# Performance work log

Measured on AMD Instinct MI355X. Metric: run time of the kernel, lower is better.

The kernel has to match this reference:

```python
import jax, jax.numpy as jnp
import numpy as np

B, N, C, H = 2, 2048, 1024, 16
HD = C // H
FF = 2 * C


def _layernorm(x, w, b, eps=1e-5):
    mu = jnp.mean(x, axis=-1, keepdims=True)
    var = jnp.var(x, axis=-1, keepdims=True)
    return (x - mu) * jax.lax.rsqrt(var + eps) * w + b


def setup_inputs() -> dict:
    key = jax.random.key(0)
    ks = jax.random.split(key, 16)
    std = 0.02
    d = {
        'q': jax.random.normal(ks[0], (B, N, C), jnp.float32),
        'k': jax.random.normal(ks[1], (B, N, C), jnp.float32),
        'v': jax.random.normal(ks[2], (B, N, C), jnp.float32),
        # attention projections (stored [in, out])
        'Wq': jax.random.normal(ks[3], (C, C), jnp.float32) * std,
        'bq': jnp.zeros((C,), jnp.float32),
        'Wk': jax.random.normal(ks[4], (C, C), jnp.float32) * std,
        'bk': jnp.zeros((C,), jnp.float32),
        'Wv': jax.random.normal(ks[5], (C, C), jnp.float32) * std,
        'bv': jnp.zeros((C,), jnp.float32),
        'Wo': jax.random.normal(ks[6], (C, C), jnp.float32) * std,
        'bo': jnp.zeros((C,), jnp.float32),
        # post-attention LayerNorm
        'ln_w': jnp.ones((C,), jnp.float32),
        'ln_b': jnp.zeros((C,), jnp.float32),
        # FFN
        'W1': jax.random.normal(ks[7], (C, FF), jnp.float32) * std,
        'b1': jnp.zeros((FF,), jnp.float32),
        'W2': jax.random.normal(ks[8], (FF, C), jnp.float32) * std,
        'b2': jnp.zeros((C,), jnp.float32),
    }
    return d


def reference(q, k, v, Wq, bq, Wk, bk, Wv, bv, Wo, bo, ln_w, ln_b, W1, b1, W2, b2):
    scale = HD ** -0.5
    # Note: the torch forward overwrites the normalized-input attention with
    # attention on raw q,k,v; only the second call affects the output.
    qh = (q @ Wq + bq).reshape(B, N, H, HD)  # [B,Nq,H,hd]
    kh = (k @ Wk + bk).reshape(B, N, H, HD)
    vh = (v @ Wv + bv).reshape(B, N, H, HD)
    attn = jnp.einsum('bqhd,bkhd->bhqk', qh, kh) * scale
    attn = jax.nn.softmax(attn, axis=-1)
    ctx = jnp.einsum('bhqk,bkhd->bqhd', attn, vh).reshape(B, N, C)
    x = ctx @ Wo + bo
    x = x + q  # residual (drop_path=0, dropout eval -> identity)
    h = _layernorm(x, ln_w, ln_b)
    y = jax.nn.gelu(h @ W1 + b1, approximate=False) @ W2 + b2
    return y + x
```

## Files before the change

### kernel.cpp

```cpp
#include <hip/hip_runtime.h>

constexpr int B_ = 2, N_ = 2048, C_ = 1024, H_ = 16, HD_ = 64, FF_ = 2048;

typedef __attribute__((ext_vector_type(8))) __bf16 bf16x8;
typedef __attribute__((ext_vector_type(4))) float f32x4;
typedef __attribute__((ext_vector_type(4))) short s16x4;

__device__ __forceinline__ unsigned short f2bf(float f) {
  union { float f; unsigned int u; } v; v.f = f;
  unsigned int r = v.u + 0x7fffu + ((v.u >> 16) & 1u);
  return (unsigned short)(r >> 16);
}

__device__ __forceinline__ void gload_lds16(const unsigned short* g, unsigned short* l) {
  __builtin_amdgcn_global_load_lds((const __attribute__((address_space(1))) void*)g,
                                   (__attribute__((address_space(3))) void*)l, 16, 0, 0);
}

__global__ __launch_bounds__(256)
void cast3_bf16(const float* __restrict__ q, const float* __restrict__ k,
                const float* __restrict__ v, unsigned short* __restrict__ qo,
                unsigned short* __restrict__ ko, unsigned short* __restrict__ vo, int n8) {
  int i = blockIdx.x * 256 + threadIdx.x;
  if (i >= n8) return;
  const float* in = blockIdx.z == 0 ? q : (blockIdx.z == 1 ? k : v);
  unsigned short* out = blockIdx.z == 0 ? qo : (blockIdx.z == 1 ? ko : vo);
  const float4 a = ((const float4*)in)[2 * i];
  const float4 b = ((const float4*)in)[2 * i + 1];
  uint4 o;
  o.x = (unsigned)f2bf(a.x) | ((unsigned)f2bf(a.y) << 16);
  o.y = (unsigned)f2bf(a.z) | ((unsigned)f2bf(a.w) << 16);
  o.z = (unsigned)f2bf(b.x) | ((unsigned)f2bf(b.y) << 16);
  o.w = (unsigned)f2bf(b.z) | ((unsigned)f2bf(b.w) << 16);
  ((uint4*)out)[i] = o;
}

__global__ __launch_bounds__(256)
void wt_cast(const float* __restrict__ W, unsigned short* __restrict__ Wt, int K, int N) {
  __shared__ unsigned short tile[32][33];
  const int tx = threadIdx.x, ty = threadIdx.y;
  const int n0 = blockIdx.x * 32, k0 = blockIdx.y * 32;
#pragma unroll
  for (int r = 0; r < 4; ++r)
    tile[ty + r * 8][tx] = f2bf(W[(size_t)(k0 + ty + r * 8) * N + n0 + tx]);
  __syncthreads();
#pragma unroll
  for (int r = 0; r < 4; ++r)
    Wt[(size_t)(n0 + ty + r * 8) * K + k0 + tx] = tile[tx][ty + r * 8];
}

__global__ __launch_bounds__(256)
void wt_cast4(const float* __restrict__ Wa, const float* __restrict__ Wb,
              const float* __restrict__ Wc, const float* __restrict__ Wd,
              unsigned short* __restrict__ Oa, unsigned short* __restrict__ Ob,
              unsigned short* __restrict__ Oc, unsigned short* __restrict__ Od) {
  __shared__ unsigned short tile[32][33];
  const int z = blockIdx.z;
  const float* W = z == 0 ? Wa : (z == 1 ? Wb : (z == 2 ? Wc : Wd));
  unsigned short* Wt = z == 0 ? Oa : (z == 1 ? Ob : (z == 2 ? Oc : Od));
  const int tx = threadIdx.x, ty = threadIdx.y;
  const int n0 = blockIdx.x * 32, k0 = blockIdx.y * 32;
#pragma unroll
  for (int r = 0; r < 4; ++r)
    tile[ty + r * 8][tx] = f2bf(W[(size_t)(k0 + ty + r * 8) * C_ + n0 + tx]);
  __syncthreads();
#pragma unroll
  for (int r = 0; r < 4; ++r)
    Wt[(size_t)(n0 + ty + r * 8) * C_ + k0 + tx] = tile[tx][ty + r * 8];
}

__global__ __launch_bounds__(256)
void vh_transpose(const unsigned short* __restrict__ Vh, unsigned short* __restrict__ VhT) {
  __shared__ unsigned short tile[32][33];
  const int tx = threadIdx.x, ty = threadIdx.y;
  const int bh = blockIdx.z, b = bh >> 4, h = bh & 15;
  const int n0 = blockIdx.x * 32, d0 = blockIdx.y * 32;
#pragma unroll
  for (int r = 0; r < 4; ++r) {
    int n = n0 + ty + r * 8;
    tile[ty + r * 8][tx] = Vh[((size_t)(b * N_ + n)) * C_ + h * HD_ + d0 + tx];
  }
  __syncthreads();
#pragma unroll
  for (int r = 0; r < 4; ++r) {
    int d = d0 + ty + r * 8;
    VhT[((size_t)(bh * HD_ + d)) * N_ + n0 + tx] = tile[tx][ty + r * 8];
  }
}

__global__ __launch_bounds__(256, 2)
void gemm_qkv(const unsigned short* __restrict__ A0, const unsigned short* __restrict__ A1,
              const unsigned short* __restrict__ A2, const unsigned short* __restrict__ B0,
              const unsigned short* __restrict__ B1, const unsigned short* __restrict__ B2,
              const float* __restrict__ c0, const float* __restrict__ c1v,
              const float* __restrict__ c2, unsigned short* __restrict__ O0,
              unsigned short* __restrict__ O1, unsigned short* __restrict__ O2) {
  const int z = blockIdx.z;
  const unsigned short* A = z == 0 ? A0 : (z == 1 ? A1 : A2);
  const unsigned short* Bt = z == 0 ? B0 : (z == 1 ? B1 : B2);
  const float* bias = z == 0 ? c0 : (z == 1 ? c1v : c2);
  unsigned short* outB = z == 0 ? O0 : (z == 1 ? O1 : O2);
  const int K = C_, Nn = C_;

  __shared__ unsigned short lA[2][128 * 64];
  __shared__ unsigned short lB[2][128 * 64];
  const int t = threadIdx.x;
  const int lane = t & 63;
  const int w = t >> 6;
  const int wm = w >> 1, wn = w & 1;
  const int l15 = lane & 15, g = lane >> 4;

  const unsigned short* Ab = A + (size_t)blockIdx.x * 128 * K;
  const unsigned short* Bb = Bt + (size_t)blockIdx.y * 128 * K;

  auto stage = [&](int buf, int k0) {
#pragma unroll
    for (int i = 0; i < 4; ++i) {
      int id = i * 256 + t;
      gload_lds16(Ab + (size_t)(id >> 3) * K + k0 + (id & 7) * 8, &lA[buf][id * 8]);
    }
#pragma unroll
    for (int i = 0; i < 4; ++i) {
      int id = i * 256 + t;
      gload_lds16(Bb + (size_t)(id >> 3) * K + k0 + (id & 7) * 8, &lB[buf][id * 8]);
    }
  };

  f32x4 acc[4][4] = {};

  stage(0, 0);
  __syncthreads();
  int cur = 0;
  for (int k0 = 0; k0 < K; k0 += 64) {
    if (k0 + 64 < K) stage(cur ^ 1, k0 + 64);
#pragma unroll
    for (int kk = 0; kk < 2; ++kk) {
      bf16x8 af[4], bfr[4];
#pragma unroll
      for (int mi = 0; mi < 4; ++mi)
        af[mi] = *(const bf16x8*)&lA[cur][(wm * 64 + mi * 16 + l15) * 64 + kk * 32 + g * 8];
#pragma unroll
      for (int ni = 0; ni < 4; ++ni)
        bfr[ni] = *(const bf16x8*)&lB[cur][(wn * 64 + ni * 16 + l15) * 64 + kk * 32 + g * 8];
      __builtin_amdgcn_s_setprio(1);
#pragma unroll
      for (int mi = 0; mi < 4; ++mi)
#pragma unroll
        for (int ni = 0; ni < 4; ++ni)
          acc[mi][ni] = __builtin_amdgcn_mfma_f32_16x16x32_bf16(af[mi], bfr[ni], acc[mi][ni], 0, 0, 0);
      __builtin_amdgcn_s_setprio(0);
    }
    __syncthreads();
    cur ^= 1;
  }

#pragma unroll
  for (int mi = 0; mi < 4; ++mi)
#pragma unroll
    for (int ni = 0; ni < 4; ++ni) {
      const int col = blockIdx.y * 128 + wn * 64 + ni * 16 + l15;
      const float bcol = bias[col];
#pragma unroll
      for (int r = 0; r < 4; ++r) {
        const int row = blockIdx.x * 128 + wm * 64 + mi * 16 + g * 4 + r;
        outB[(size_t)row * Nn + col] = f2bf(acc[mi][ni][r] + bcol);
      }
    }
}

template <int EPI>
__global__ __launch_bounds__(256, 2)
void gemm_bt(const unsigned short* __restrict__ A, const unsigned short* __restrict__ Bt,
             const float* __restrict__ bias, const float* __restrict__ resid,
             float* __restrict__ outF, unsigned short* __restrict__ outB,
             int M, int N, int K) {
  __shared__ unsigned short lA[2][128 * 64];
  __shared__ unsigned short lB[2][128 * 64];
  const int t = threadIdx.x;
  const int lane = t & 63;
  const int w = t >> 6;
  const int wm = w >> 1, wn = w & 1;
  const int l15 = lane & 15, g = lane >> 4;

  const unsigned short* Ab = A + (size_t)blockIdx.x * 128 * K;
  const unsigned short* Bb = Bt + (size_t)blockIdx.y * 128 * K;

  auto stage = [&](int buf, int k0) {
#pragma unroll
    for (int i = 0; i < 4; ++i) {
      int id = i * 256 + t;
      gload_lds16(Ab + (size_t)(id >> 3) * K + k0 + (id & 7) * 8, &lA[buf][id * 8]);
    }
#pragma unroll
    for (int i = 0; i < 4; ++i) {
      int id = i * 256 + t;
      gload_lds16(Bb + (size_t)(id >> 3) * K + k0 + (id & 7) * 8, &lB[buf][id * 8]);
    }
  };

  f32x4 acc[4][4] = {};

  stage(0, 0);
  __syncthreads();
  int cur = 0;
  for (int k0 = 0; k0 < K; k0 += 64) {
    if (k0 + 64 < K) stage(cur ^ 1, k0 + 64);
#pragma unroll
    for (int kk = 0; kk < 2; ++kk) {
      bf16x8 af[4], bfr[4];
#pragma unroll
      for (int mi = 0; mi < 4; ++mi)
        af[mi] = *(const bf16x8*)&lA[cur][(wm * 64 + mi * 16 + l15) * 64 + kk * 32 + g * 8];
#pragma unroll
      for (int ni = 0; ni < 4; ++ni)
        bfr[ni] = *(const bf16x8*)&lB[cur][(wn * 64 + ni * 16 + l15) * 64 + kk * 32 + g * 8];
      __builtin_amdgcn_s_setprio(1);
#pragma unroll
      for (int mi = 0; mi < 4; ++mi)
#pragma unroll
        for (int ni = 0; ni < 4; ++ni)
          acc[mi][ni] = __builtin_amdgcn_mfma_f32_16x16x32_bf16(af[mi], bfr[ni], acc[mi][ni], 0, 0, 0);
      __builtin_amdgcn_s_setprio(0);
    }
    __syncthreads();
    cur ^= 1;
  }

#pragma unroll
  for (int mi = 0; mi < 4; ++mi)
#pragma unroll
    for (int ni = 0; ni < 4; ++ni) {
      const int col = blockIdx.y * 128 + wn * 64 + ni * 16 + l15;
      const float bcol = bias[col];
#pragma unroll
      for (int r = 0; r < 4; ++r) {
        const int row = blockIdx.x * 128 + wm * 64 + mi * 16 + g * 4 + r;
        const size_t o = (size_t)row * N + col;
        float val = acc[mi][ni][r] + bcol;
        if (EPI == 0) {
          outB[o] = f2bf(val);
        } else if (EPI == 1) {
          outF[o] = val + resid[o];
        } else {
          float ge = 0.5f * val * (1.0f + erff(val * 0.70710678118654752f));
          outB[o] = f2bf(ge);
        }
      }
    }
}

__global__ __launch_bounds__(256, 2)
void gemm_n64(const unsigned short* __restrict__ A, const unsigned short* __restrict__ Bt,
              const float* __restrict__ bias, const float* __restrict__ resid,
              float* __restrict__ outF, int M, int N, int K) {
  __shared__ unsigned short lA[2][128 * 64];
  __shared__ unsigned short lB[2][64 * 64];
  const int t = threadIdx.x;
  const int lane = t & 63;
  const int w = t >> 6;
  const int wm = w >> 1, wn = w & 1;
  const int l15 = lane & 15, g = lane >> 4;

  const unsigned short* Ab = A + (size_t)blockIdx.x * 128 * K;
  const unsigned short* Bb = Bt + (size_t)blockIdx.y * 64 * K;

  auto stage = [&](int buf, int k0) {
#pragma unroll
    for (int i = 0; i < 4; ++i) {
      int id = i * 256 + t;
      gload_lds16(Ab + (size_t)(id >> 3) * K + k0 + (id & 7) * 8, &lA[buf][id * 8]);
    }
#pragma unroll
    for (int i = 0; i < 2; ++i) {
      int id = i * 256 + t;
      gload_lds16(Bb + (size_t)(id >> 3) * K + k0 + (id & 7) * 8, &lB[buf][id * 8]);
    }
  };

  f32x4 acc[4][2] = {};

  stage(0, 0);
  __syncthreads();
  int cur = 0;
  for (int k0 = 0; k0 < K; k0 += 64) {
    if (k0 + 64 < K) stage(cur ^ 1, k0 + 64);
#pragma unroll
    for (int kk = 0; kk < 2; ++kk) {
      bf16x8 af[4], bfr[2];
#pragma unroll
      for (int mi = 0; mi < 4; ++mi)
        af[mi] = *(const bf16x8*)&lA[cur][(wm * 64 + mi * 16 + l15) * 64 + kk * 32 + g * 8];
#pragma unroll
      for (int ni = 0; ni < 2; ++ni)
        bfr[ni] = *(const bf16x8*)&lB[cur][(wn * 32 + ni * 16 + l15) * 64 + kk * 32 + g * 8];
      __builtin_amdgcn_s_setprio(1);
#pragma unroll
      for (int mi = 0; mi < 4; ++mi)
#pragma unroll
        for (int ni = 0; ni < 2; ++ni)
          acc[mi][ni] = __builtin_amdgcn_mfma_f32_16x16x32_bf16(af[mi], bfr[ni], acc[mi][ni], 0, 0, 0);
      __builtin_amdgcn_s_setprio(0);
    }
    __syncthreads();
    cur ^= 1;
  }

#pragma unroll
  for (int mi = 0; mi < 4; ++mi)
#pragma unroll
    for (int ni = 0; ni < 2; ++ni) {
      const int col = blockIdx.y * 64 + wn * 32 + ni * 16 + l15;
      const float bcol = bias[col];
#pragma unroll
      for (int r = 0; r < 4; ++r) {
        const int row = blockIdx.x * 128 + wm * 64 + mi * 16 + g * 4 + r;
        const size_t o = (size_t)row * N + col;
        outF[o] = acc[mi][ni][r] + bcol + resid[o];
      }
    }
}

__global__ __launch_bounds__(512, 2)
void attn_fwd(const unsigned short* __restrict__ Qh, const unsigned short* __restrict__ Kh,
              const unsigned short* __restrict__ VhT, unsigned short* __restrict__ ctx) {
  __shared__ unsigned short lK[2][64 * 64];
  __shared__ unsigned short lV[2][64 * 64];

  const int t = threadIdx.x, lane = t & 63, w = t >> 6;
  const int l15 = lane & 15, g = lane >> 4;
  const int bh = blockIdx.y, b = bh >> 4, h = bh & 15;
  const int qb0 = blockIdx.x * 256 + w * 32;

  const unsigned short* Qb = Qh + (size_t)b * N_ * C_ + h * HD_;
  const unsigned short* Kb = Kh + (size_t)b * N_ * C_ + h * HD_;
  const unsigned short* Vb = VhT + (size_t)bh * HD_ * N_;

  bf16x8 qf[2][2];
#pragma unroll
  for (int qi = 0; qi < 2; ++qi)
#pragma unroll
    for (int kk = 0; kk < 2; ++kk)
      qf[qi][kk] = *(const bf16x8*)(Qb + (size_t)(qb0 + qi * 16 + l15) * C_ + kk * 32 + g * 8);

  auto stageK = [&](int buf, int kb) {
    int o = t * 16;
    int r = o >> 7;
    int c = (o & 127) ^ ((r & 7) << 4);
    gload_lds16(Kb + (size_t)(kb + r) * C_ + (c >> 1), &lK[buf][o >> 1]);
  };
  auto stageV = [&](int buf, int kb) {
    int o = t * 16;
    int r = o >> 7;
    int c = (o & 127) ^ ((r & 7) << 4);
    gload_lds16(Vb + (size_t)r * N_ + kb + (c >> 1), &lV[buf][o >> 1]);
  };

  f32x4 od[4][2] = {};
  float mrun[2] = {-1e30f, -1e30f};
  float srun[2] = {0.f, 0.f};
  const float c1 = 0.18033688011112042f;
  const float DTHR = 8.0f / 0.18033688011112042f;

  stageK(0, 0);
  stageV(0, 0);
  __syncthreads();

  int cur = 0;
  for (int tile = 0; tile < N_ / 64; ++tile) {
    if (tile + 1 < N_ / 64) {
      stageK(cur ^ 1, (tile + 1) * 64);
      stageV(cur ^ 1, (tile + 1) * 64);
    }

    f32x4 st[4][2];
    __builtin_amdgcn_s_setprio(1);
#pragma unroll
    for (int kf = 0; kf < 4; ++kf) {
      const int krow = kf * 16 + l15;
      const int sw = (krow & 7) << 4;
      const bf16x8 ka = *(const bf16x8*)&lK[cur][krow * 64 + ((( g * 16) ^ sw) >> 1)];
      const bf16x8 kc = *(const bf16x8*)&lK[cur][krow * 64 + (((64 + g * 16) ^ sw) >> 1)];
#pragma unroll
      for (int qi = 0; qi < 2; ++qi) {
        f32x4 z = {};
        z = __builtin_amdgcn_mfma_f32_16x16x32_bf16(ka, qf[qi][0], z, 0, 0, 0);
        z = __builtin_amdgcn_mfma_f32_16x16x32_bf16(kc, qf[qi][1], z, 0, 0, 0);
        st[kf][qi] = z;
      }
    }
    __builtin_amdgcn_s_setprio(0);

    s16x4 pb[4][2];
#pragma unroll
    for (int qi = 0; qi < 2; ++qi) {
      float mx = st[0][qi][0];
#pragma unroll
      for (int r = 1; r < 4; ++r) mx = fmaxf(mx, st[0][qi][r]);
#pragma unroll
      for (int kf = 1; kf < 4; ++kf)
#pragma unroll
        for (int r = 0; r < 4; ++r) mx = fmaxf(mx, st[kf][qi][r]);
      mx = fmaxf(mx, __shfl_xor(mx, 16));
      mx = fmaxf(mx, __shfl_xor(mx, 32));
      if (__any(mx > mrun[qi] + DTHR)) {
        const float mn = fmaxf(mrun[qi], mx);
        const float sf = exp2f((mrun[qi] - mn) * c1);
        mrun[qi] = mn;
        srun[qi] *= sf;
#pragma unroll
        for (int di = 0; di < 4; ++di)
#pragma unroll
          for (int r = 0; r < 4; ++r) od[di][qi][r] *= sf;
      }
      const float mc = mrun[qi] * c1;
#pragma unroll
      for (int kf = 0; kf < 4; ++kf) {
        union { s16x4 v; __bf16 e[4]; } u;
#pragma unroll
        for (int r = 0; r < 4; ++r) {
          float pv = exp2f(st[kf][qi][r] * c1 - mc);
          srun[qi] += pv;
          u.e[r] = (__bf16)pv;
        }
        pb[kf][qi] = u.v;
      }
    }

    __builtin_amdgcn_s_setprio(1);
#pragma unroll
    for (int di = 0; di < 4; ++di) {
      const int vrow = di * 16 + l15;
      const int sw = (vrow & 7) << 4;
#pragma unroll
      for (int kf = 0; kf < 4; ++kf) {
        const s16x4 vt = *(const s16x4*)&lV[cur][vrow * 64 + (((kf * 32 + g * 8) ^ sw) >> 1)];
#pragma unroll
        for (int qi = 0; qi < 2; ++qi)
          od[di][qi] = __builtin_amdgcn_mfma_f32_16x16x16bf16_1k(vt, pb[kf][qi], od[di][qi], 0, 0, 0);
      }
    }
    __builtin_amdgcn_s_setprio(0);

    __syncthreads();
    cur ^= 1;
  }

#pragma unroll
  for (int qi = 0; qi < 2; ++qi) {
    float s = srun[qi];
    s += __shfl_xor(s, 16);
    s += __shfl_xor(s, 32);
    const float rinv = 1.0f / s;
    const int q = qb0 + qi * 16 + l15;
    unsigned short* cp = ctx + ((size_t)(b * N_ + q)) * C_ + h * HD_;
#pragma unroll
    for (int di = 0; di < 4; ++di) {
      uint2 o;
      o.x = (unsigned)f2bf(od[di][qi][0] * rinv) | ((unsigned)f2bf(od[di][qi][1] * rinv) << 16);
      o.y = (unsigned)f2bf(od[di][qi][2] * rinv) | ((unsigned)f2bf(od[di][qi][3] * rinv) << 16);
      *(uint2*)(cp + di * 16 + g * 4) = o;
    }
  }
}

__global__ __launch_bounds__(256)
void ln_kernel(const float* __restrict__ x, const float* __restrict__ lw,
               const float* __restrict__ lb, unsigned short* __restrict__ h) {
  const int row = blockIdx.x;
  const int t = threadIdx.x;
  const float4 v = ((const float4*)(x + (size_t)row * C_))[t];
  float sum = v.x + v.y + v.z + v.w;
#pragma unroll
  for (int m = 1; m < 64; m <<= 1) sum += __shfl_xor(sum, m);
  __shared__ float red[8];
  if ((t & 63) == 0) red[t >> 6] = sum;
  __syncthreads();
  const float mu = (red[0] + red[1] + red[2] + red[3]) * (1.0f / C_);
  const float d0 = v.x - mu, d1 = v.y - mu, d2 = v.z - mu, d3 = v.w - mu;
  float sq = d0 * d0 + d1 * d1 + d2 * d2 + d3 * d3;
#pragma unroll
  for (int m = 1; m < 64; m <<= 1) sq += __shfl_xor(sq, m);
  if ((t & 63) == 0) red[4 + (t >> 6)] = sq;
  __syncthreads();
  const float var = (red[4] + red[5] + red[6] + red[7]) * (1.0f / C_);
  const float rstd = rsqrtf(var + 1e-5f);
  const float4 ww = ((const float4*)lw)[t];
  const float4 bb = ((const float4*)lb)[t];
  uint2 o;
  o.x = (unsigned)f2bf(d0 * rstd * ww.x + bb.x) | ((unsigned)f2bf(d1 * rstd * ww.y + bb.y) << 16);
  o.y = (unsigned)f2bf(d2 * rstd * ww.z + bb.z) | ((unsigned)f2bf(d3 * rstd * ww.w + bb.w) << 16);
  ((uint2*)(h + (size_t)row * C_))[t] = o;
}

extern "C" void kernel_launch(void* const* d_in, const int* in_sizes, int n_in,
                              void* d_out, int out_size, void* d_ws, size_t ws_size,
                              hipStream_t stream) {
  const float* q   = (const float*)d_in[0];
  const float* k   = (const float*)d_in[1];
  const float* v   = (const float*)d_in[2];
  const float* Wq  = (const float*)d_in[3];
  const float* bq  = (const float*)d_in[4];
  const float* Wk  = (const float*)d_in[5];
  const float* bk  = (const float*)d_in[6];
  const float* Wv  = (const float*)d_in[7];
  const float* bv  = (const float*)d_in[8];
  const float* Wo  = (const float*)d_in[9];
  const float* bo  = (const float*)d_in[10];
  const float* lnw = (const float*)d_in[11];
  const float* lnb = (const float*)d_in[12];
  const float* W1  = (const float*)d_in[13];
  const float* b1  = (const float*)d_in[14];
  const float* W2  = (const float*)d_in[15];
  const float* b2  = (const float*)d_in[16];
  float* out = (float*)d_out;

  char* ws = (char*)d_ws;
  const size_t MB = 1024 * 1024;
  if (ws_size < 120 * MB) return;
  unsigned short* qb   = (unsigned short*)(ws + 0 * MB);
  unsigned short* kb   = (unsigned short*)(ws + 8 * MB);
  unsigned short* vb   = (unsigned short*)(ws + 16 * MB);
  unsigned short* Wqt  = (unsigned short*)(ws + 24 * MB);
  unsigned short* Wkt  = (unsigned short*)(ws + 26 * MB);
  unsigned short* Wvt  = (unsigned short*)(ws + 28 * MB);
  unsigned short* Wot  = (unsigned short*)(ws + 30 * MB);
  unsigned short* W1t  = (unsigned short*)(ws + 32 * MB);
  unsigned short* W2t  = (unsigned short*)(ws + 36 * MB);
  unsigned short* Qh   = (unsigned short*)(ws + 40 * MB);
  unsigned short* Kh   = (unsigned short*)(ws + 48 * MB);
  unsigned short* Vh   = (unsigned short*)(ws + 56 * MB);
  unsigned short* VhT  = (unsigned short*)(ws + 64 * MB);
  unsigned short* ctx  = (unsigned short*)(ws + 72 * MB);
  float*          xf   = (float*)(ws + 80 * MB);
  unsigned short* hb   = (unsigned short*)(ws + 96 * MB);
  unsigned short* tbuf = (unsigned short*)(ws + 104 * MB);

  const int n8 = B_ * N_ * C_ / 8;
  cast3_bf16<<<dim3((n8 + 255) / 256, 1, 3), 256, 0, stream>>>(q, k, v, qb, kb, vb, n8);

  dim3 blk32(32, 8);
  wt_cast4<<<dim3(C_ / 32, C_ / 32, 4), blk32, 0, stream>>>(Wq, Wk, Wv, Wo, Wqt, Wkt, Wvt, Wot);
  wt_cast<<<dim3(FF_ / 32, C_ / 32), blk32, 0, stream>>>(W1, W1t, C_, FF_);
  wt_cast<<<dim3(C_ / 32, FF_ / 32), blk32, 0, stream>>>(W2, W2t, FF_, C_);

  gemm_qkv<<<dim3(B_ * N_ / 128, C_ / 128, 3), 256, 0, stream>>>(qb, kb, vb, Wqt, Wkt, Wvt,
                                                                 bq, bk, bv, Qh, Kh, Vh);

  vh_transpose<<<dim3(N_ / 32, HD_ / 32, B_ * H_), blk32, 0, stream>>>(Vh, VhT);
  attn_fwd<<<dim3(N_ / 256, B_ * H_), 512, 0, stream>>>(Qh, Kh, VhT, ctx);

  gemm_n64<<<dim3(B_ * N_ / 128, C_ / 64), 256, 0, stream>>>(ctx, Wot, bo, q, xf, B_ * N_, C_, C_);
  ln_kernel<<<dim3(B_ * N_), 256, 0, stream>>>(xf, lnw, lnb, hb);
  gemm_bt<2><<<dim3(B_ * N_ / 128, FF_ / 128), 256, 0, stream>>>(hb, W1t, b1, nullptr, nullptr, tbuf,
                                                                 B_ * N_, FF_, C_);
  gemm_n64<<<dim3(B_ * N_ / 128, C_ / 64), 256, 0, stream>>>(tbuf, W2t, b2, xf, out, B_ * N_, C_, FF_);
}
```

Measured before the change: 251.5 us.

## Split attention over key halves with merge kernel and fold scale into Q

Attention now splits the key sequence into two halves via a grid z dimension, with each warp handling 16 query rows instead of 32. Each split writes unnormalized fp32 partial outputs plus running max and sum, and a new merge kernel combines them into bf16 ctx. The softmax scale times log2e is folded into the Q projection epilogue, which removes per-element multiplies in the softmax. The goal is more blocks and occupancy for attention, at the cost of extra fp32 partial traffic, an extra launch, halved K/V reuse per block, and a reshuffled workspace layout.

```diff
diff --git a/kernel.cpp b/kernel.cpp
--- a/kernel.cpp
+++ b/kernel.cpp
@@ -100,6 +100,7 @@
   const unsigned short* Bt = z == 0 ? B0 : (z == 1 ? B1 : B2);
   const float* bias = z == 0 ? c0 : (z == 1 ? c1v : c2);
   unsigned short* outB = z == 0 ? O0 : (z == 1 ? O1 : O2);
+  const float sc = z == 0 ? 0.18033688011112042f : 1.0f;
   const int K = C_, Nn = C_;
 
   __shared__ unsigned short lA[2][128 * 64];
@@ -163,7 +164,7 @@
 #pragma unroll
       for (int r = 0; r < 4; ++r) {
         const int row = blockIdx.x * 128 + wm * 64 + mi * 16 + g * 4 + r;
-        outB[(size_t)row * Nn + col] = f2bf(acc[mi][ni][r] + bcol);
+        outB[(size_t)row * Nn + col] = f2bf((acc[mi][ni][r] + bcol) * sc);
       }
     }
 }
@@ -320,27 +321,29 @@
     }
 }
 
-__global__ __launch_bounds__(512, 2)
+__global__ __launch_bounds__(512, 8)
 void attn_fwd(const unsigned short* __restrict__ Qh, const unsigned short* __restrict__ Kh,
-              const unsigned short* __restrict__ VhT, unsigned short* __restrict__ ctx) {
+              const unsigned short* __restrict__ VhT, float* __restrict__ odp,
+              float* __restrict__ mlp) {
   __shared__ unsigned short lK[2][64 * 64];
   __shared__ unsigned short lV[2][64 * 64];
 
   const int t = threadIdx.x, lane = t & 63, w = t >> 6;
   const int l15 = lane & 15, g = lane >> 4;
   const int bh = blockIdx.y, b = bh >> 4, h = bh & 15;
-  const int qb0 = blockIdx.x * 256 + w * 32;
+  const int sp = blockIdx.z;
+  const int qb0 = blockIdx.x * 128 + w * 16;
+  const int kbase = sp * (N_ / 2);
+  const int NT = (N_ / 2) / 64;
 
   const unsigned short* Qb = Qh + (size_t)b * N_ * C_ + h * HD_;
   const unsigned short* Kb = Kh + (size_t)b * N_ * C_ + h * HD_;
   const unsigned short* Vb = VhT + (size_t)bh * HD_ * N_;
 
-  bf16x8 qf[2][2];
-#pragma unroll
-  for (int qi = 0; qi < 2; ++qi)
-#pragma unroll
-    for (int kk = 0; kk < 2; ++kk)
-      qf[qi][kk] = *(const bf16x8*)(Qb + (size_t)(qb0 + qi * 16 + l15) * C_ + kk * 32 + g * 8);
+  bf16x8 qf[2];
+#pragma unroll
+  for (int kk = 0; kk < 2; ++kk)
+    qf[kk] = *(const bf16x8*)(Qb + (size_t)(qb0 + l15) * C_ + kk * 32 + g * 8);
 
   auto stageK = [&](int buf, int kb) {
     int o = t * 16;
@@ -355,24 +358,23 @@
     gload_lds16(Vb + (size_t)r * N_ + kb + (c >> 1), &lV[buf][o >> 1]);
   };
 
-  f32x4 od[4][2] = {};
-  float mrun[2] = {-1e30f, -1e30f};
-  float srun[2] = {0.f, 0.f};
-  const float c1 = 0.18033688011112042f;
-  const float DTHR = 8.0f / 0.18033688011112042f;
-
-  stageK(0, 0);
-  stageV(0, 0);
+  f32x4 od[4] = {};
+  float mrun = -1e30f;
+  float srun = 0.f;
+  const float DTHR = 11.541560327111707f;
+
+  stageK(0, kbase);
+  stageV(0, kbase);
   __syncthreads();
 
   int cur = 0;
-  for (int tile = 0; tile < N_ / 64; ++tile) {
-    if (tile + 1 < N_ / 64) {
-      stageK(cur ^ 1, (tile + 1) * 64);
-      stageV(cur ^ 1, (tile + 1) * 64);
-    }
-
-    f32x4 st[4][2];
+  for (int tile = 0; tile < NT; ++tile) {
+    if (tile + 1 < NT) {
+      stageK(cur ^ 1, kbase + (tile + 1) * 64);
+      stageV(cur ^ 1, kbase + (tile + 1) * 64);
+    }
+
+    f32x4 st[4];
     __builtin_amdgcn_s_setprio(1);
 #pragma unroll
     for (int kf = 0; kf < 4; ++kf) {
@@ -380,50 +382,43 @@
       const int sw = (krow & 7) << 4;
       const bf16x8 ka = *(const bf16x8*)&lK[cur][krow * 64 + ((( g * 16) ^ sw) >> 1)];
       const bf16x8 kc = *(const bf16x8*)&lK[cur][krow * 64 + (((64 + g * 16) ^ sw) >> 1)];
-#pragma unroll
-      for (int qi = 0; qi < 2; ++qi) {
-        f32x4 z = {};
-        z = __builtin_amdgcn_mfma_f32_16x16x32_bf16(ka, qf[qi][0], z, 0, 0, 0);
-        z = __builtin_amdgcn_mfma_f32_16x16x32_bf16(kc, qf[qi][1], z, 0, 0, 0);
-        st[kf][qi] = z;
+      f32x4 z = {};
+      z = __builtin_amdgcn_mfma_f32_16x16x32_bf16(ka, qf[0], z, 0, 0, 0);
+      z = __builtin_amdgcn_mfma_f32_16x16x32_bf16(kc, qf[1], z, 0, 0, 0);
+      st[kf] = z;
+    }
+    __builtin_amdgcn_s_setprio(0);
+
+    float mx = st[0][0];
+#pragma unroll
+    for (int r = 1; r < 4; ++r) mx = fmaxf(mx, st[0][r]);
+#pragma unroll
+    for (int kf = 1; kf < 4; ++kf)
+#pragma unroll
+      for (int r = 0; r < 4; ++r) mx = fmaxf(mx, st[kf][r]);
+    mx = fmaxf(mx, __shfl_xor(mx, 16));
+    mx = fmaxf(mx, __shfl_xor(mx, 32));
+    if (__any(mx > mrun + DTHR)) {
+      const float mn = fmaxf(mrun, mx);
+      const float sf = exp2f(mrun - mn);
+      mrun = mn;
+      srun *= sf;
+#pragma unroll
+      for (int di = 0; di < 4; ++di)
+#pragma unroll
+        for (int r = 0; r < 4; ++r) od[di][r] *= sf;
+    }
+    s16x4 pb[4];
+#pragma unroll
+    for (int kf = 0; kf < 4; ++kf) {
+      union { s16x4 v; __bf16 e[4]; } u;
+#pragma unroll
+      for (int r = 0; r < 4; ++r) {
+        float pv = exp2f(st[kf][r] - mrun);
+        srun += pv;
+        u.e[r] = (__bf16)pv;
       }
-    }
-    __builtin_amdgcn_s_setprio(0);
-
-    s16x4 pb[4][2];
-#pragma unroll
-    for (int qi = 0; qi < 2; ++qi) {
-      float mx = st[0][qi][0];
-#pragma unroll
-      for (int r = 1; r < 4; ++r) mx = fmaxf(mx, st[0][qi][r]);
-#pragma unroll
-      for (int kf = 1; kf < 4; ++kf)
-#pragma unroll
-        for (int r = 0; r < 4; ++r) mx = fmaxf(mx, st[kf][qi][r]);
-      mx = fmaxf(mx, __shfl_xor(mx, 16));
-      mx = fmaxf(mx, __shfl_xor(mx, 32));
-      if (__any(mx > mrun[qi] + DTHR)) {
-        const float mn = fmaxf(mrun[qi], mx);
-        const float sf = exp2f((mrun[qi] - mn) * c1);
-        mrun[qi] = mn;
-        srun[qi] *= sf;
-#pragma unroll
-        for (int di = 0; di < 4; ++di)
-#pragma unroll
-          for (int r = 0; r < 4; ++r) od[di][qi][r] *= sf;
-      }
-      const float mc = mrun[qi] * c1;
-#pragma unroll
-      for (int kf = 0; kf < 4; ++kf) {
-        union { s16x4 v; __bf16 e[4]; } u;
-#pragma unroll
-        for (int r = 0; r < 4; ++r) {
-          float pv = exp2f(st[kf][qi][r] * c1 - mc);
-          srun[qi] += pv;
-          u.e[r] = (__bf16)pv;
-        }
-        pb[kf][qi] = u.v;
-      }
+      pb[kf] = u.v;
     }
 
     __builtin_amdgcn_s_setprio(1);
@@ -434,9 +429,7 @@
 #pragma unroll
       for (int kf = 0; kf < 4; ++kf) {
         const s16x4 vt = *(const s16x4*)&lV[cur][vrow * 64 + (((kf * 32 + g * 8) ^ sw) >> 1)];
-#pragma unroll
-        for (int qi = 0; qi < 2; ++qi)
-          od[di][qi] = __builtin_amdgcn_mfma_f32_16x16x16bf16_1k(vt, pb[kf][qi], od[di][qi], 0, 0, 0);
+        od[di] = __builtin_amdgcn_mfma_f32_16x16x16bf16_1k(vt, pb[kf], od[di], 0, 0, 0);
       }
     }
     __builtin_amdgcn_s_setprio(0);
@@ -445,22 +438,40 @@
     cur ^= 1;
   }
 
-#pragma unroll
-  for (int qi = 0; qi < 2; ++qi) {
-    float s = srun[qi];
-    s += __shfl_xor(s, 16);
-    s += __shfl_xor(s, 32);
-    const float rinv = 1.0f / s;
-    const int q = qb0 + qi * 16 + l15;
-    unsigned short* cp = ctx + ((size_t)(b * N_ + q)) * C_ + h * HD_;
-#pragma unroll
-    for (int di = 0; di < 4; ++di) {
-      uint2 o;
-      o.x = (unsigned)f2bf(od[di][qi][0] * rinv) | ((unsigned)f2bf(od[di][qi][1] * rinv) << 16);
-      o.y = (unsigned)f2bf(od[di][qi][2] * rinv) | ((unsigned)f2bf(od[di][qi][3] * rinv) << 16);
-      *(uint2*)(cp + di * 16 + g * 4) = o;
-    }
-  }
+  float s = srun;
+  s += __shfl_xor(s, 16);
+  s += __shfl_xor(s, 32);
+  const int q = qb0 + l15;
+  const size_t row = (size_t)sp * B_ * N_ + (size_t)b * N_ + q;
+  float* op = odp + row * C_ + h * HD_;
+#pragma unroll
+  for (int di = 0; di < 4; ++di)
+    *(f32x4*)(op + di * 16 + g * 4) = od[di];
+  if (g == 0) {
+    float2 ml = {mrun, s};
+    *(float2*)(mlp + (row * H_ + h) * 2) = ml;
+  }
+}
+
+__global__ __launch_bounds__(256)
+void attn_merge(const float* __restrict__ odp, const float* __restrict__ mlp,
+                unsigned short* __restrict__ ctx) {
+  const int row = blockIdx.x;
+  const int t = threadIdx.x;
+  const int h = t >> 4, d0 = (t & 15) * 4;
+  const size_t half = (size_t)B_ * N_;
+  const float2 ml1 = *(const float2*)(mlp + ((size_t)row * H_ + h) * 2);
+  const float2 ml2 = *(const float2*)(mlp + ((half + row) * H_ + h) * 2);
+  const float M = fmaxf(ml1.x, ml2.x);
+  float a1 = exp2f(ml1.x - M), a2 = exp2f(ml2.x - M);
+  const float rL = 1.0f / (ml1.y * a1 + ml2.y * a2);
+  a1 *= rL; a2 *= rL;
+  const float4 o1 = *(const float4*)(odp + (size_t)row * C_ + h * 64 + d0);
+  const float4 o2 = *(const float4*)(odp + (half + row) * C_ + h * 64 + d0);
+  uint2 o;
+  o.x = (unsigned)f2bf(o1.x * a1 + o2.x * a2) | ((unsigned)f2bf(o1.y * a1 + o2.y * a2) << 16);
+  o.y = (unsigned)f2bf(o1.z * a1 + o2.z * a2) | ((unsigned)f2bf(o1.w * a1 + o2.w * a2) << 16);
+  *(uint2*)(ctx + (size_t)row * C_ + h * 64 + d0) = o;
 }
 
 __global__ __launch_bounds__(256)
@@ -520,20 +531,22 @@
   unsigned short* qb   = (unsigned short*)(ws + 0 * MB);
   unsigned short* kb   = (unsigned short*)(ws + 8 * MB);
   unsigned short* vb   = (unsigned short*)(ws + 16 * MB);
-  unsigned short* Wqt  = (unsigned short*)(ws + 24 * MB);
-  unsigned short* Wkt  = (unsigned short*)(ws + 26 * MB);
-  unsigned short* Wvt  = (unsigned short*)(ws + 28 * MB);
-  unsigned short* Wot  = (unsigned short*)(ws + 30 * MB);
-  unsigned short* W1t  = (unsigned short*)(ws + 32 * MB);
-  unsigned short* W2t  = (unsigned short*)(ws + 36 * MB);
-  unsigned short* Qh   = (unsigned short*)(ws + 40 * MB);
-  unsigned short* Kh   = (unsigned short*)(ws + 48 * MB);
-  unsigned short* Vh   = (unsigned short*)(ws + 56 * MB);
-  unsigned short* VhT  = (unsigned short*)(ws + 64 * MB);
-  unsigned short* ctx  = (unsigned short*)(ws + 72 * MB);
-  float*          xf   = (float*)(ws + 80 * MB);
-  unsigned short* hb   = (unsigned short*)(ws + 96 * MB);
-  unsigned short* tbuf = (unsigned short*)(ws + 104 * MB);
+  float*          odp  = (float*)(ws + 0 * MB);
+  float*          mlp  = (float*)(ws + 32 * MB);
+  unsigned short* tbuf = (unsigned short*)(ws + 0 * MB);
+  unsigned short* hb   = (unsigned short*)(ws + 16 * MB);
+  unsigned short* Wqt  = (unsigned short*)(ws + 33 * MB);
+  unsigned short* Wkt  = (unsigned short*)(ws + 35 * MB);
+  unsigned short* Wvt  = (unsigned short*)(ws + 37 * MB);
+  unsigned short* Wot  = (unsigned short*)(ws + 39 * MB);
+  unsigned short* W1t  = (unsigned short*)(ws + 41 * MB);
+  unsigned short* W2t  = (unsigned short*)(ws + 45 * MB);
+  unsigned short* Qh   = (unsigned short*)(ws + 49 * MB);
+  unsigned short* Kh   = (unsigned short*)(ws + 57 * MB);
+  unsigned short* Vh   = (unsigned short*)(ws + 65 * MB);
+  unsigned short* VhT  = (unsigned short*)(ws + 73 * MB);
+  unsigned short* ctx  = (unsigned short*)(ws + 81 * MB);
+  float*          xf   = (float*)(ws + 89 * MB);
 
   const int n8 = B_ * N_ * C_ / 8;
   cast3_bf16<<<dim3((n8 + 255) / 256, 1, 3), 256, 0, stream>>>(q, k, v, qb, kb, vb, n8);
@@ -547,7 +560,8 @@
                                                                  bq, bk, bv, Qh, Kh, Vh);
 
   vh_transpose<<<dim3(N_ / 32, HD_ / 32, B_ * H_), blk32, 0, stream>>>(Vh, VhT);
-  attn_fwd<<<dim3(N_ / 256, B_ * H_), 512, 0, stream>>>(Qh, Kh, VhT, ctx);
+  attn_fwd<<<dim3(N_ / 128, B_ * H_, 2), 512, 0, stream>>>(Qh, Kh, VhT, odp, mlp);
+  attn_merge<<<dim3(B_ * N_), 256, 0, stream>>>(odp, mlp, ctx);
 
   gemm_n64<<<dim3(B_ * N_ / 128, C_ / 64), 256, 0, stream>>>(ctx, Wot, bo, q, xf, B_ * N_, C_, C_);
   ln_kernel<<<dim3(B_ * N_), 256, 0, stream>>>(xf, lnw, lnb, hb);
```

Result: slower. 264.4 us (+5.2%).
